# Kernel tuning notes

Hardware: AMD Instinct MI355X
Metric: run time of the kernel (lower is better)

The kernel has to match this reference:

```python
import jax, jax.numpy as jnp
import numpy as np

NUM_NODES = 256
INPUTS = list(range(8))
OUTPUTS = list(range(248, 256))
V_MEAS = np.array(sorted(set(range(NUM_NODES)) - set(OUTPUTS)))  # 0..247
V_CORR = np.array(sorted(set(range(NUM_NODES)) - set(INPUTS)))   # 8..255
INNER_LR = 0.1
INNER_ITER = 200
B1, B2, ADAM_EPS = 0.9, 0.999, 1e-8
CAUSAL_EPS = 0.1


def _parity_loss(G, A_sub):
    # G, A_sub: [B, m, c]; enforces sum(A*G) odd
    S = jnp.sum(A_sub * G, axis=2)                 # [B, m]
    val = jnp.sin(jnp.pi * S / 2) ** 2
    return jnp.mean((val - 1.0) ** 2)


def _causal_loss(G, T):
    # T: [B, n]; penalty = relu(T_u - T_v + eps)
    T_u = T[:, V_MEAS][:, :, None]                 # [B, m, 1]
    T_v = T[:, V_CORR][:, None, :]                 # [B, 1, c]
    penalty = jax.nn.relu(T_u - T_v + CAUSAL_EPS)  # [B, m, c]
    return jnp.mean(G * penalty)


def setup_inputs() -> dict:
    key = jax.random.key(0)
    k1, k2, k3 = jax.random.split(key, 3)
    B = 128
    adj_batch = jax.random.uniform(k1, (B, NUM_NODES, NUM_NODES), dtype=jnp.float32)
    G_logits0 = jax.random.normal(k2, (B, len(V_MEAS), len(V_CORR)), dtype=jnp.float32)
    T0 = jax.random.uniform(k3, (B, NUM_NODES), dtype=jnp.float32)
    return {"adj_batch": adj_batch, "G_logits0": G_logits0, "T0": T0}


def reference(adj_batch, G_logits0, T0):
    A_sub = adj_batch[:, V_MEAS][:, :, V_CORR]     # [B, m, c]
    A_det = jax.lax.stop_gradient(A_sub)           # adj is detached in the inner loop

    def inner_loss(params):
        G_logits, T = params
        G = jax.nn.sigmoid(G_logits)
        loss_p = _parity_loss(G, A_det)
        loss_c = _causal_loss(G, T)
        loss_s = jnp.mean(jnp.abs(G - 0.5)) * 0.1
        return loss_p + loss_c + loss_s

    grad_fn = jax.grad(inner_loss)

    def adam_step(carry, t):
        params, m, v = carry
        g = grad_fn(params)
        m = jax.tree.map(lambda m_, g_: B1 * m_ + (1 - B1) * g_, m, g)
        v = jax.tree.map(lambda v_, g_: B2 * v_ + (1 - B2) * g_ * g_, v, g)
        bc1 = 1.0 - B1 ** t
        bc2 = 1.0 - B2 ** t
        params = jax.tree.map(
            lambda p, m_, v_: p - INNER_LR * (m_ / bc1) / (jnp.sqrt(v_ / bc2) + ADAM_EPS),
            params, m, v)
        return (params, m, v), None

    params0 = (G_logits0, T0)
    zeros = jax.tree.map(jnp.zeros_like, params0)
    steps = jnp.arange(1, INNER_ITER + 1, dtype=jnp.float32)
    (params, _, _), _ = jax.lax.scan(adam_step, (params0, zeros, zeros), steps)

    G_logits, T = jax.lax.stop_gradient(params)    # .detach() in torch source
    G_final = jax.nn.sigmoid(G_logits)
    final_parity = _parity_loss(G_final, A_sub)    # differentiable w.r.t. adj_batch
    final_causal = _causal_loss(G_final, T)
    return (final_parity + final_causal, final_parity, final_causal)
```

## Files before the change

### kernel.cpp

```cpp
#include <hip/hip_runtime.h>
#include <math.h>

#define B_N   128
#define M_N   248
#define C_N   248
#define NODES 256
#define NBLK  8
#define RPB   31
#define NG    (B_N*M_N*C_N)
#define NT    (B_N*NODES)

#define PI_F     3.14159265358979323846f
#define INV_BM   (1.0f/31744.0f)
#define INV_BMC  (1.0f/7872512.0f)

__device__ __forceinline__ float sigm(float x) {
    float z = expf(-fabsf(x));
    return (x >= 0.0f) ? 1.0f/(1.0f+z) : z/(1.0f+z);
}

__device__ __forceinline__ float sgn(float x) {
    return (x > 0.0f) ? 1.0f : ((x < 0.0f) ? -1.0f : 0.0f);
}

__global__ __launch_bounds__(256) void iter_kernel(
    const float* __restrict__ adj, float* __restrict__ Gl,
    float* __restrict__ mG, float* __restrict__ vG,
    float* __restrict__ T_state, float* __restrict__ mT, float* __restrict__ vT,
    float* __restrict__ gTu, float* __restrict__ gTv,
    int t, float bc1p, float bc2p, float bc1, float bc2)
{
    __shared__ float T_lds[NODES];
    __shared__ float gv_lds[4*NODES];
    const int tid = threadIdx.x;
    const int b   = blockIdx.x >> 3;
    const int blk = blockIdx.x & 7;

    if (t == 1) {
        T_lds[tid] = T_state[b*NODES + tid];
    } else {
        const int rs = t & 1, ws2 = (t+1) & 1, ps = (t-1) & 1;
        const int idx = b*NODES + tid;
        float Tval = T_state[rs*NT + idx];
        float g = 0.0f;
        if (tid < M_N) g += gTu[ps*(B_N*M_N) + b*M_N + tid];
        if (tid >= 8) {
            const float* gp = gTv + (size_t)ps*(B_N*NBLK*C_N) + (size_t)b*NBLK*C_N + (tid-8);
            float s = 0.0f;
            #pragma unroll
            for (int k = 0; k < NBLK; ++k) s += gp[k*C_N];
            g -= s;
        }
        g *= INV_BMC;
        float m_ = 0.9f*mT[rs*NT+idx] + 0.1f*g;
        float v_ = 0.999f*vT[rs*NT+idx] + 0.001f*(g*g);
        float newT = Tval - 0.1f*(m_/bc1p)/(sqrtf(v_/bc2p) + 1e-8f);
        T_state[ws2*NT+idx] = newT;
        mT[ws2*NT+idx] = m_;
        vT[ws2*NT+idx] = v_;
        T_lds[tid] = newT;
    }
    gv_lds[tid] = 0.0f; gv_lds[256+tid] = 0.0f; gv_lds[512+tid] = 0.0f; gv_lds[768+tid] = 0.0f;
    __syncthreads();

    const int wave = tid >> 6, lane = tid & 63;
    const int pw = t & 1;
    const int j0 = lane, j1 = lane+64, j2 = lane+128, j3 = lane+192;
    const bool v3 = (lane < 56);
    float av0 = 0.0f, av1 = 0.0f, av2 = 0.0f, av3 = 0.0f;

    for (int r = wave; r < RPB; r += 4) {
        const int i = blk*RPB + r;
        const size_t arow = ((size_t)(b*NODES + i))*NODES + 8;
        const size_t grow = ((size_t)(b*M_N + i))*C_N;

        float gl0 = Gl[grow+j0], gl1 = Gl[grow+j1], gl2 = Gl[grow+j2];
        float gl3 = v3 ? Gl[grow+j3] : 0.0f;
        float a0 = adj[arow+j0], a1 = adj[arow+j1], a2 = adj[arow+j2];
        float a3 = v3 ? adj[arow+j3] : 0.0f;
        float G0 = sigm(gl0), G1 = sigm(gl1), G2 = sigm(gl2), G3 = sigm(gl3);

        float Tu = T_lds[i];
        float d0 = Tu - T_lds[j0+8] + 0.1f;
        float d1 = Tu - T_lds[j1+8] + 0.1f;
        float d2 = Tu - T_lds[j2+8] + 0.1f;
        float d3 = v3 ? (Tu - T_lds[j3+8] + 0.1f) : 0.0f;
        float p0 = fmaxf(d0, 0.0f), p1 = fmaxf(d1, 0.0f);
        float p2 = fmaxf(d2, 0.0f), p3 = fmaxf(d3, 0.0f);
        float mk0 = (d0 > 0.0f) ? 1.0f : 0.0f;
        float mk1 = (d1 > 0.0f) ? 1.0f : 0.0f;
        float mk2 = (d2 > 0.0f) ? 1.0f : 0.0f;
        float mk3 = (v3 && d3 > 0.0f) ? 1.0f : 0.0f;

        float sp = a0*G0 + a1*G1 + a2*G2 + (v3 ? a3*G3 : 0.0f);
        float gu = G0*mk0 + G1*mk1 + G2*mk2 + G3*mk3;
        #pragma unroll
        for (int off = 32; off > 0; off >>= 1) {
            sp += __shfl_xor(sp, off, 64);
            gu += __shfl_xor(gu, off, 64);
        }
        av0 += G0*mk0; av1 += G1*mk1; av2 += G2*mk2; av3 += G3*mk3;

        float half_arg = (PI_F*sp)*0.5f;
        float sv = sinf(half_arg), cv = cosf(half_arg);
        float val = sv*sv;
        float coefP = 2.0f*(val-1.0f)*sv*cv*PI_F*INV_BM;

        if (lane == 0) gTu[pw*(B_N*M_N) + b*M_N + i] = gu;

        #define DO_SLOT(Gx, glx, ax, px, jx, valid) do { if (valid) {            \
            float dG  = coefP*(ax) + (px)*INV_BMC + 0.1f*INV_BMC*sgn((Gx)-0.5f); \
            float grd = dG * (Gx) * (1.0f - (Gx));                               \
            float m_ = 0.9f*mG[grow+(jx)] + 0.1f*grd;                            \
            float v_ = 0.999f*vG[grow+(jx)] + 0.001f*(grd*grd);                  \
            mG[grow+(jx)] = m_; vG[grow+(jx)] = v_;                              \
            Gl[grow+(jx)] = (glx) - 0.1f*(m_/bc1)/(sqrtf(v_/bc2)+1e-8f);         \
        } } while (0)
        DO_SLOT(G0, gl0, a0, p0, j0, true);
        DO_SLOT(G1, gl1, a1, p1, j1, true);
        DO_SLOT(G2, gl2, a2, p2, j2, true);
        DO_SLOT(G3, gl3, a3, p3, j3, v3);
        #undef DO_SLOT
    }

    gv_lds[wave*256 + j0] = av0;
    gv_lds[wave*256 + j1] = av1;
    gv_lds[wave*256 + j2] = av2;
    if (v3) gv_lds[wave*256 + j3] = av3;
    __syncthreads();
    if (tid < C_N) {
        float s = gv_lds[tid] + gv_lds[256+tid] + gv_lds[512+tid] + gv_lds[768+tid];
        gTv[(size_t)pw*(B_N*NBLK*C_N) + (size_t)(b*NBLK + blk)*C_N + tid] = s;
    }
}

__global__ __launch_bounds__(256) void t_fin_kernel(
    float* __restrict__ T_state, const float* __restrict__ mT, const float* __restrict__ vT,
    const float* __restrict__ gTu, const float* __restrict__ gTv,
    float bc1p, float bc2p)
{
    const int b = blockIdx.x, tid = threadIdx.x;
    const int idx = b*NODES + tid;
    float Tval = T_state[1*NT + idx];
    float g = 0.0f;
    if (tid < M_N) g += gTu[0*(B_N*M_N) + b*M_N + tid];
    if (tid >= 8) {
        const float* gp = gTv + (size_t)b*NBLK*C_N + (tid-8);
        float s = 0.0f;
        #pragma unroll
        for (int k = 0; k < NBLK; ++k) s += gp[k*C_N];
        g -= s;
    }
    g *= INV_BMC;
    float m_ = 0.9f*mT[1*NT+idx] + 0.1f*g;
    float v_ = 0.999f*vT[1*NT+idx] + 0.001f*(g*g);
    T_state[0*NT+idx] = Tval - 0.1f*(m_/bc1p)/(sqrtf(v_/bc2p) + 1e-8f);
}

__global__ __launch_bounds__(256) void loss_kernel(
    const float* __restrict__ adj, const float* __restrict__ Gl,
    const float* __restrict__ T_state, float* __restrict__ accum)
{
    __shared__ float T_lds[NODES];
    __shared__ float red[8];
    const int tid = threadIdx.x;
    const int b = blockIdx.x >> 3, blk = blockIdx.x & 7;
    T_lds[tid] = T_state[b*NODES + tid];
    __syncthreads();
    const int wave = tid >> 6, lane = tid & 63;
    const int j0 = lane, j1 = lane+64, j2 = lane+128, j3 = lane+192;
    const bool v3 = (lane < 56);
    float pacc = 0.0f, cacc = 0.0f;

    for (int r = wave; r < RPB; r += 4) {
        const int i = blk*RPB + r;
        const size_t arow = ((size_t)(b*NODES + i))*NODES + 8;
        const size_t grow = ((size_t)(b*M_N + i))*C_N;
        float gl0 = Gl[grow+j0], gl1 = Gl[grow+j1], gl2 = Gl[grow+j2];
        float gl3 = v3 ? Gl[grow+j3] : 0.0f;
        float a0 = adj[arow+j0], a1 = adj[arow+j1], a2 = adj[arow+j2];
        float a3 = v3 ? adj[arow+j3] : 0.0f;
        float G0 = sigm(gl0), G1 = sigm(gl1), G2 = sigm(gl2), G3 = sigm(gl3);

        float Tu = T_lds[i];
        float p0 = fmaxf(Tu - T_lds[j0+8] + 0.1f, 0.0f);
        float p1 = fmaxf(Tu - T_lds[j1+8] + 0.1f, 0.0f);
        float p2 = fmaxf(Tu - T_lds[j2+8] + 0.1f, 0.0f);
        float p3 = v3 ? fmaxf(Tu - T_lds[j3+8] + 0.1f, 0.0f) : 0.0f;

        float sp = a0*G0 + a1*G1 + a2*G2 + (v3 ? a3*G3 : 0.0f);
        float cp = G0*p0 + G1*p1 + G2*p2 + (v3 ? G3*p3 : 0.0f);
        #pragma unroll
        for (int off = 32; off > 0; off >>= 1) {
            sp += __shfl_xor(sp, off, 64);
            cp += __shfl_xor(cp, off, 64);
        }
        if (lane == 0) {
            float sv = sinf((PI_F*sp)*0.5f);
            float dd = sv*sv - 1.0f;
            pacc += dd*dd;
            cacc += cp;
        }
    }
    if (lane == 0) { red[wave] = pacc; red[4+wave] = cacc; }
    __syncthreads();
    if (tid == 0) {
        atomicAdd(&accum[0], red[0]+red[1]+red[2]+red[3]);
        atomicAdd(&accum[1], red[4]+red[5]+red[6]+red[7]);
    }
}

__global__ void finish_kernel(const float* __restrict__ accum, float* __restrict__ out) {
    if (threadIdx.x == 0 && blockIdx.x == 0) {
        float p = accum[0] / 31744.0f;
        float c = accum[1] / 7872512.0f;
        out[0] = p + c;
        out[1] = p;
        out[2] = c;
    }
}

extern "C" void kernel_launch(void* const* d_in, const int* in_sizes, int n_in,
                              void* d_out, int out_size, void* d_ws, size_t ws_size,
                              hipStream_t stream) {
    const float* adj = (const float*)d_in[0];
    float* Gl        = (float*)d_in[1];
    const float* T0  = (const float*)d_in[2];
    float* out       = (float*)d_out;
    float* ws        = (float*)d_ws;

    float* mG      = ws;
    float* vG      = mG + NG;
    float* T_state = vG + NG;
    float* mT      = T_state + 2*NT;
    float* vT      = mT + 2*NT;
    float* gTu     = vT + 2*NT;
    float* gTv     = gTu + 2*B_N*M_N;
    float* accum   = gTv + (size_t)2*B_N*NBLK*C_N;

    hipMemsetAsync(mG, 0, (size_t)2*NG*sizeof(float), stream);
    hipMemsetAsync(mT, 0, (size_t)4*NT*sizeof(float), stream);
    hipMemsetAsync(accum, 0, 2*sizeof(float), stream);
    hipMemcpyAsync(T_state, T0, NT*sizeof(float), hipMemcpyDeviceToDevice, stream);

    for (int t = 1; t <= 200; ++t) {
        float bc1p = 1.0f - (float)pow(0.9,   (double)(t-1));
        float bc2p = 1.0f - (float)pow(0.999, (double)(t-1));
        float bc1  = 1.0f - (float)pow(0.9,   (double)t);
        float bc2  = 1.0f - (float)pow(0.999, (double)t);
        iter_kernel<<<dim3(B_N*NBLK), dim3(256), 0, stream>>>(
            adj, Gl, mG, vG, T_state, mT, vT, gTu, gTv, t, bc1p, bc2p, bc1, bc2);
    }
    {
        float bc1p = 1.0f - (float)pow(0.9,   200.0);
        float bc2p = 1.0f - (float)pow(0.999, 200.0);
        t_fin_kernel<<<dim3(B_N), dim3(256), 0, stream>>>(T_state, mT, vT, gTu, gTv, bc1p, bc2p);
    }
    loss_kernel<<<dim3(B_N*NBLK), dim3(256), 0, stream>>>(adj, Gl, T_state, accum);
    finish_kernel<<<1, 64, 0, stream>>>(accum, out);
}
```

Before: 8.169 ms.

## Fuse Adam loop into persistent cooperative kernel with register-resident G state

Replaces 200 per-iteration launches with a single cooperative persistent kernel of 256 blocks, each covering half of one batch's rows. The G logits and their Adam moments stay in registers, and T state lives in LDS, so the large mG/vG/G arrays are no longer streamed through HBM every step. Cross-block T gradients are exchanged through global buffers with grid.sync each iteration. This trades launch overhead and state traffic for heavy register pressure (up to 192 floats per thread, which may spill) and a grid-wide barrier per step. The old multi-launch path is kept as a fallback when co-residency is not possible.

```diff
diff --git a/kernel.cpp b/kernel.cpp
--- a/kernel.cpp
+++ b/kernel.cpp
@@ -1,14 +1,20 @@
 #include <hip/hip_runtime.h>
+#include <hip/hip_cooperative_groups.h>
 #include <math.h>
+
+namespace cg = cooperative_groups;
 
 #define B_N   128
 #define M_N   248
 #define C_N   248
 #define NODES 256
-#define NBLK  8
-#define RPB   31
+#define NT    (B_N*NODES)
 #define NG    (B_N*M_N*C_N)
-#define NT    (B_N*NODES)
+
+#define GRID  256
+#define TPB   512
+#define HROWS 124
+#define KMAX  16
 
 #define PI_F     3.14159265358979323846f
 #define INV_BM   (1.0f/31744.0f)
@@ -18,10 +24,221 @@
     float z = expf(-fabsf(x));
     return (x >= 0.0f) ? 1.0f/(1.0f+z) : z/(1.0f+z);
 }
-
 __device__ __forceinline__ float sgn(float x) {
     return (x > 0.0f) ? 1.0f : ((x < 0.0f) ? -1.0f : 0.0f);
 }
+
+__global__ __launch_bounds__(TPB, 2) void persist_kernel(
+    const float* __restrict__ adj, const float* __restrict__ Gl0,
+    const float* __restrict__ T0,
+    float* __restrict__ gTu,
+    float* __restrict__ gTv,
+    float* __restrict__ accum,
+    float* __restrict__ out)
+{
+    __shared__ float T_lds[NODES], mT_lds[NODES], vT_lds[NODES];
+    __shared__ float red[16];
+
+    cg::grid_group grid = cg::this_grid();
+    const int tid  = threadIdx.x;
+    const int blkI = blockIdx.x;
+    const int b    = blkI >> 1;
+    const int h    = blkI & 1;
+    const int wave = tid >> 6, lane = tid & 63;
+    const int j0 = lane, j1 = lane+64, j2 = lane+128, j3 = lane+192;
+    const bool v3 = (lane < 56);
+
+    if (tid < NODES) {
+        T_lds[tid]  = T0[b*NODES + tid];
+        mT_lds[tid] = 0.0f;
+        vT_lds[tid] = 0.0f;
+    }
+
+    float Gr[KMAX][4], mGr[KMAX][4], vGr[KMAX][4];
+    #pragma unroll
+    for (int k = 0; k < KMAX; ++k) {
+        #pragma unroll
+        for (int s = 0; s < 4; ++s) { Gr[k][s]=0.0f; mGr[k][s]=0.0f; vGr[k][s]=0.0f; }
+        const int lr = wave + 8*k;
+        if (lr < HROWS) {
+            const int i = h*HROWS + lr;
+            const size_t grow = ((size_t)(b*M_N + i))*C_N;
+            Gr[k][0] = Gl0[grow+j0];
+            Gr[k][1] = Gl0[grow+j1];
+            Gr[k][2] = Gl0[grow+j2];
+            if (v3) Gr[k][3] = Gl0[grow+j3];
+        }
+    }
+    __syncthreads();
+
+    double pw1d = 1.0, pw2d = 1.0;
+    #pragma unroll 1
+    for (int t = 1; t <= 200; ++t) {
+        const float bc1p = (float)(1.0 - pw1d), bc2p = (float)(1.0 - pw2d);
+        pw1d *= 0.9; pw2d *= 0.999;
+        const float bc1 = (float)(1.0 - pw1d), bc2 = (float)(1.0 - pw2d);
+        const int pw = t & 1, ps = (t-1) & 1;
+
+        if (t > 1) {
+            grid.sync();
+            if (tid < NODES) {
+                float g = 0.0f;
+                if (tid < M_N) g += gTu[ps*(B_N*M_N) + b*M_N + tid];
+                if (tid >= 8) {
+                    const float* gp = gTv + (size_t)ps*(GRID*8*256)
+                                    + (size_t)(b*16)*256 + (tid-8);
+                    float s = 0.0f;
+                    #pragma unroll
+                    for (int p = 0; p < 16; ++p) s += gp[p*256];
+                    g -= s;
+                }
+                g *= INV_BMC;
+                float m_ = 0.9f*mT_lds[tid] + 0.1f*g;
+                float v_ = 0.999f*vT_lds[tid] + 0.001f*(g*g);
+                mT_lds[tid] = m_; vT_lds[tid] = v_;
+                T_lds[tid] = T_lds[tid] - 0.1f*(m_/bc1p)/(sqrtf(v_/bc2p) + 1e-8f);
+            }
+            __syncthreads();
+        }
+
+        float av0 = 0.0f, av1 = 0.0f, av2 = 0.0f, av3 = 0.0f;
+        #pragma unroll
+        for (int k = 0; k < KMAX; ++k) {
+            const int lr = wave + 8*k;
+            if (lr < HROWS) {
+                const int i = h*HROWS + lr;
+                const size_t arow = ((size_t)(b*NODES + i))*NODES + 8;
+                const float a0 = adj[arow+j0];
+                const float a1 = adj[arow+j1];
+                const float a2 = adj[arow+j2];
+                const float a3 = v3 ? adj[arow+j3] : 0.0f;
+
+                const float G0 = sigm(Gr[k][0]), G1 = sigm(Gr[k][1]);
+                const float G2 = sigm(Gr[k][2]), G3 = sigm(Gr[k][3]);
+
+                const float Tu = T_lds[i];
+                const float d0 = Tu - T_lds[j0+8] + 0.1f;
+                const float d1 = Tu - T_lds[j1+8] + 0.1f;
+                const float d2 = Tu - T_lds[j2+8] + 0.1f;
+                const float d3 = v3 ? (Tu - T_lds[j3+8] + 0.1f) : 0.0f;
+                const float p0 = fmaxf(d0,0.0f), p1 = fmaxf(d1,0.0f);
+                const float p2 = fmaxf(d2,0.0f), p3 = fmaxf(d3,0.0f);
+                const float mk0 = (d0>0.0f)?1.0f:0.0f;
+                const float mk1 = (d1>0.0f)?1.0f:0.0f;
+                const float mk2 = (d2>0.0f)?1.0f:0.0f;
+                const float mk3 = (v3 && d3>0.0f)?1.0f:0.0f;
+
+                float sp = a0*G0 + a1*G1 + a2*G2 + (v3 ? a3*G3 : 0.0f);
+                float gu = G0*mk0 + G1*mk1 + G2*mk2 + G3*mk3;
+                #pragma unroll
+                for (int off = 32; off > 0; off >>= 1) {
+                    sp += __shfl_xor(sp, off, 64);
+                    gu += __shfl_xor(gu, off, 64);
+                }
+                av0 += G0*mk0; av1 += G1*mk1; av2 += G2*mk2; av3 += G3*mk3;
+
+                const float half_arg = (PI_F*sp)*0.5f;
+                const float sv = sinf(half_arg), cv = cosf(half_arg);
+                const float coefP = 2.0f*(sv*sv-1.0f)*sv*cv*PI_F*INV_BM;
+
+                if (lane == 0) gTu[pw*(B_N*M_N) + b*M_N + i] = gu;
+
+                #define DO_SLOT(Gx, ax, px, s_, valid) do { if (valid) {                 \
+                    float dG  = coefP*(ax) + (px)*INV_BMC + 0.1f*INV_BMC*sgn((Gx)-0.5f); \
+                    float grd = dG * (Gx) * (1.0f - (Gx));                               \
+                    float m_ = 0.9f*mGr[k][s_] + 0.1f*grd;                               \
+                    float v_ = 0.999f*vGr[k][s_] + 0.001f*(grd*grd);                     \
+                    mGr[k][s_] = m_; vGr[k][s_] = v_;                                    \
+                    Gr[k][s_] = Gr[k][s_] - 0.1f*(m_/bc1)/(sqrtf(v_/bc2)+1e-8f);         \
+                } } while (0)
+                DO_SLOT(G0, a0, p0, 0, true);
+                DO_SLOT(G1, a1, p1, 1, true);
+                DO_SLOT(G2, a2, p2, 2, true);
+                DO_SLOT(G3, a3, p3, 3, v3);
+                #undef DO_SLOT
+            }
+        }
+        {
+            float* gpw = gTv + (size_t)pw*(GRID*8*256) + (size_t)(blkI*8 + wave)*256;
+            gpw[j0] = av0; gpw[j1] = av1; gpw[j2] = av2; gpw[j3] = av3;
+        }
+    }
+
+    grid.sync();
+    if (tid < NODES) {
+        const float bc1p = (float)(1.0 - pw1d), bc2p = (float)(1.0 - pw2d);
+        float g = 0.0f;
+        if (tid < M_N) g += gTu[0*(B_N*M_N) + b*M_N + tid];
+        if (tid >= 8) {
+            const float* gp = gTv + (size_t)(b*16)*256 + (tid-8);
+            float s = 0.0f;
+            #pragma unroll
+            for (int p = 0; p < 16; ++p) s += gp[p*256];
+            g -= s;
+        }
+        g *= INV_BMC;
+        float m_ = 0.9f*mT_lds[tid] + 0.1f*g;
+        float v_ = 0.999f*vT_lds[tid] + 0.001f*(g*g);
+        T_lds[tid] = T_lds[tid] - 0.1f*(m_/bc1p)/(sqrtf(v_/bc2p) + 1e-8f);
+    }
+    __syncthreads();
+
+    float pacc = 0.0f, cacc = 0.0f;
+    #pragma unroll
+    for (int k = 0; k < KMAX; ++k) {
+        const int lr = wave + 8*k;
+        if (lr < HROWS) {
+            const int i = h*HROWS + lr;
+            const size_t arow = ((size_t)(b*NODES + i))*NODES + 8;
+            const float a0 = adj[arow+j0];
+            const float a1 = adj[arow+j1];
+            const float a2 = adj[arow+j2];
+            const float a3 = v3 ? adj[arow+j3] : 0.0f;
+            const float G0 = sigm(Gr[k][0]), G1 = sigm(Gr[k][1]);
+            const float G2 = sigm(Gr[k][2]), G3 = sigm(Gr[k][3]);
+            const float Tu = T_lds[i];
+            const float p0 = fmaxf(Tu - T_lds[j0+8] + 0.1f, 0.0f);
+            const float p1 = fmaxf(Tu - T_lds[j1+8] + 0.1f, 0.0f);
+            const float p2 = fmaxf(Tu - T_lds[j2+8] + 0.1f, 0.0f);
+            const float p3 = v3 ? fmaxf(Tu - T_lds[j3+8] + 0.1f, 0.0f) : 0.0f;
+
+            float sp = a0*G0 + a1*G1 + a2*G2 + (v3 ? a3*G3 : 0.0f);
+            float cp = G0*p0 + G1*p1 + G2*p2 + (v3 ? G3*p3 : 0.0f);
+            #pragma unroll
+            for (int off = 32; off > 0; off >>= 1) {
+                sp += __shfl_xor(sp, off, 64);
+                cp += __shfl_xor(cp, off, 64);
+            }
+            if (lane == 0) {
+                const float sv = sinf((PI_F*sp)*0.5f);
+                const float dd = sv*sv - 1.0f;
+                pacc += dd*dd;
+                cacc += cp;
+            }
+        }
+    }
+    if (lane == 0) { red[wave] = pacc; red[8+wave] = cacc; }
+    __syncthreads();
+    if (tid == 0) {
+        float rp = 0.0f, rc = 0.0f;
+        #pragma unroll
+        for (int w = 0; w < 8; ++w) { rp += red[w]; rc += red[8+w]; }
+        atomicAdd(&accum[0], rp);
+        atomicAdd(&accum[1], rc);
+    }
+    __threadfence();
+    grid.sync();
+    if (blkI == 0 && tid == 0) {
+        const float p = __hip_atomic_load(&accum[0], __ATOMIC_RELAXED, __HIP_MEMORY_SCOPE_AGENT) * INV_BM;
+        const float c = __hip_atomic_load(&accum[1], __ATOMIC_RELAXED, __HIP_MEMORY_SCOPE_AGENT) * INV_BMC;
+        out[0] = p + c;
+        out[1] = p;
+        out[2] = c;
+    }
+}
+
+#define NBLK  8
+#define RPB   31
 
 __global__ __launch_bounds__(256) void iter_kernel(
     const float* __restrict__ adj, float* __restrict__ Gl,
@@ -229,33 +446,53 @@
     float* out       = (float*)d_out;
     float* ws        = (float*)d_ws;
 
-    float* mG      = ws;
-    float* vG      = mG + NG;
-    float* T_state = vG + NG;
-    float* mT      = T_state + 2*NT;
-    float* vT      = mT + 2*NT;
-    float* gTu     = vT + 2*NT;
-    float* gTv     = gTu + 2*B_N*M_N;
-    float* accum   = gTv + (size_t)2*B_N*NBLK*C_N;
-
-    hipMemsetAsync(mG, 0, (size_t)2*NG*sizeof(float), stream);
-    hipMemsetAsync(mT, 0, (size_t)4*NT*sizeof(float), stream);
-    hipMemsetAsync(accum, 0, 2*sizeof(float), stream);
-    hipMemcpyAsync(T_state, T0, NT*sizeof(float), hipMemcpyDeviceToDevice, stream);
-
-    for (int t = 1; t <= 200; ++t) {
-        float bc1p = 1.0f - (float)pow(0.9,   (double)(t-1));
-        float bc2p = 1.0f - (float)pow(0.999, (double)(t-1));
-        float bc1  = 1.0f - (float)pow(0.9,   (double)t);
-        float bc2  = 1.0f - (float)pow(0.999, (double)t);
-        iter_kernel<<<dim3(B_N*NBLK), dim3(256), 0, stream>>>(
-            adj, Gl, mG, vG, T_state, mT, vT, gTu, gTv, t, bc1p, bc2p, bc1, bc2);
-    }
-    {
-        float bc1p = 1.0f - (float)pow(0.9,   200.0);
-        float bc2p = 1.0f - (float)pow(0.999, 200.0);
-        t_fin_kernel<<<dim3(B_N), dim3(256), 0, stream>>>(T_state, mT, vT, gTu, gTv, bc1p, bc2p);
-    }
-    loss_kernel<<<dim3(B_N*NBLK), dim3(256), 0, stream>>>(adj, Gl, T_state, accum);
-    finish_kernel<<<1, 64, 0, stream>>>(accum, out);
-}
+    int dev = 0;  hipGetDevice(&dev);
+    int numCU = 0;
+    hipDeviceGetAttribute(&numCU, hipDeviceAttributeMultiprocessorCount, dev);
+    int maxB = 0;
+    hipOccupancyMaxActiveBlocksPerMultiprocessor(&maxB, persist_kernel, TPB, 0);
+    const bool coop_ok = (maxB >= 1) && ((long)maxB * (long)numCU >= GRID);
+
+    if (coop_ok) {
+        float* gTu   = ws;
+        float* gTv   = gTu + 2*B_N*M_N;
+        float* accum = gTv + (size_t)2*GRID*8*256;
+        hipMemsetAsync(accum, 0, 2*sizeof(float), stream);
+
+        const float* Gl0 = Gl;
+        void* args[] = { (void*)&adj, (void*)&Gl0, (void*)&T0,
+                         (void*)&gTu, (void*)&gTv, (void*)&accum, (void*)&out };
+        hipLaunchCooperativeKernel((void*)persist_kernel,
+                                   dim3(GRID), dim3(TPB), args, 0, stream);
+    } else {
+        float* mG      = ws;
+        float* vG      = mG + NG;
+        float* T_state = vG + NG;
+        float* mT      = T_state + 2*NT;
+        float* vT      = mT + 2*NT;
+        float* gTu     = vT + 2*NT;
+        float* gTv     = gTu + 2*B_N*M_N;
+        float* accum   = gTv + (size_t)2*B_N*NBLK*C_N;
+
+        hipMemsetAsync(mG, 0, (size_t)2*NG*sizeof(float), stream);
+        hipMemsetAsync(mT, 0, (size_t)4*NT*sizeof(float), stream);
+        hipMemsetAsync(accum, 0, 2*sizeof(float), stream);
+        hipMemcpyAsync(T_state, T0, NT*sizeof(float), hipMemcpyDeviceToDevice, stream);
+
+        for (int t = 1; t <= 200; ++t) {
+            float bc1p = 1.0f - (float)pow(0.9,   (double)(t-1));
+            float bc2p = 1.0f - (float)pow(0.999, (double)(t-1));
+            float bc1  = 1.0f - (float)pow(0.9,   (double)t);
+            float bc2  = 1.0f - (float)pow(0.999, (double)t);
+            iter_kernel<<<dim3(B_N*NBLK), dim3(256), 0, stream>>>(
+                adj, Gl, mG, vG, T_state, mT, vT, gTu, gTv, t, bc1p, bc2p, bc1, bc2);
+        }
+        {
+            float bc1p = 1.0f - (float)pow(0.9,   200.0);
+            float bc2p = 1.0f - (float)pow(0.999, 200.0);
+            t_fin_kernel<<<dim3(B_N), dim3(256), 0, stream>>>(T_state, mT, vT, gTu, gTv, bc1p, bc2p);
+        }
+        loss_kernel<<<dim3(B_N*NBLK), dim3(256), 0, stream>>>(adj, Gl, T_state, accum);
+        finish_kernel<<<1, 64, 0, stream>>>(accum, out);
+    }
+}
```

Result: no change. 8.113 ms (-0.7%).
